# Performance work log

Measured on AMD Instinct MI355X. Metric: run time of the kernel, lower is better.

The kernel has to match this reference:

```python
import jax, jax.numpy as jnp
import numpy as np

K = 16  # num neighbors


def setup_inputs() -> dict:
    key = jax.random.key(0)
    ks = jax.random.split(key, 10)
    B, N, d_in, d_out = 4, 8192, 64, 128
    h = d_out // 2
    return {
        "xyz": jax.random.normal(ks[0], (B, 3, N), jnp.float32),
        "feature": jax.random.normal(ks[1], (B, d_in, N), jnp.float32),
        "w1": jax.random.normal(ks[2], (h, 10), jnp.float32) * 0.1,
        "b1": jax.random.normal(ks[3], (h,), jnp.float32) * 0.1,
        "w2": jax.random.normal(ks[4], (h, h), jnp.float32) * 0.1,
        "b2": jax.random.normal(ks[5], (h,), jnp.float32) * 0.1,
        "w3": jax.random.normal(ks[6], (h, h), jnp.float32) * 0.1,
        "b3": jax.random.normal(ks[7], (h,), jnp.float32) * 0.1,
        "ws": jax.random.normal(ks[8], (d_out, d_in), jnp.float32) * 0.1,
        "bs": jax.random.normal(ks[9], (d_out,), jnp.float32) * 0.1,
    }


def reference(xyz, feature, w1, b1, w2, b2, w3, b3, ws, bs):
    # xyz: [B,3,N], feature: [B,d_in,N]
    xyz_t = jnp.transpose(xyz, (0, 2, 1))  # [B,N,3]
    sq = jnp.sum(xyz_t * xyz_t, axis=-1)  # [B,N]
    # squared pairwise distance [B,N,N]
    dist = sq[:, :, None] + sq[:, None, :] - 2.0 * jnp.einsum("bnc,bmc->bnm", xyz_t, xyz_t)
    _, idx = jax.lax.top_k(-dist, K)  # smallest-k -> [B,N,K]
    # gather neighbor coords: [B,N,K,3]
    knn_xyz = jax.vmap(lambda pts, ind: pts[ind])(xyz_t, idx)
    center = jnp.broadcast_to(xyz_t[:, :, None, :], knn_xyz.shape)  # [B,N,K,3]
    diff = knn_xyz - center
    dsq = jnp.sum(diff * diff, axis=-1, keepdims=True)  # [B,N,K,1]
    pos = jnp.concatenate([center, knn_xyz, diff, dsq], axis=-1)  # [B,N,K,10]
    # three 1x1 convs over channel dim (no activations, faithful to source)
    h = jnp.einsum("bnkc,oc->bnko", pos, w1) + b1
    h = jnp.einsum("bnkc,oc->bnko", h, w2) + b2
    h = jnp.einsum("bnkc,oc->bnko", h, w3) + b3
    fe = jnp.max(h, axis=2)  # max-pool over neighbors -> [B,N,d_out//2]
    fe = jnp.transpose(fe, (0, 2, 1))  # [B,d_out//2,N]
    shortcut = jnp.einsum("bcn,oc->bon", feature, ws) + bs[None, :, None]
    return jnp.concatenate([fe, fe], axis=1) + shortcut  # [B,d_out,N]
```

## Files before the change

### kernel.cpp

```cpp
#include <hip/hip_runtime.h>

#define B_ 4
#define N_ 8192
#define DIN 64
#define HDIM 64
#define DOUT 128
#define KNN 16
#define QPB 64
#define PART 8
#define NTHR (QPB * PART)
#define CHUNK (N_ / PART)
#define CAP 16
#define BLOCKS_PER_B (N_ / QPB)

__global__ __launch_bounds__(256) void k_prep(
    const float* __restrict__ xyz,
    const float* __restrict__ w1, const float* __restrict__ b1,
    const float* __restrict__ w2, const float* __restrict__ b2,
    const float* __restrict__ w3, const float* __restrict__ b3,
    float4* __restrict__ pk, float4* __restrict__ prm) {
  const int blk = blockIdx.x, t = threadIdx.x;
  const int b = blk >> 5;
  const int m = ((blk & 31) << 8) + t;
  const float* xb = xyz + (size_t)b * 3 * N_;
  float x = xb[m], y = xb[N_ + m], z = xb[2 * N_ + m];
  float sq = __fadd_rn(__fadd_rn(__fmul_rn(x, x), __fmul_rn(y, y)), __fmul_rn(z, z));
  pk[((size_t)b << 13) + m] = make_float4(x, y, z, sq);

  if (blk == 0) {
    __shared__ float M2[HDIM][10];
    __shared__ float bb[HDIM];
    const int o = t;
    if (o < HDIM) {
      float r[10];
#pragma unroll
      for (int c = 0; c < 10; c++) r[c] = 0.f;
      float s = b2[o];
      for (int l = 0; l < HDIM; l++) {
        float w = w2[o * HDIM + l];
#pragma unroll
        for (int c = 0; c < 10; c++) r[c] = fmaf(w, w1[l * 10 + c], r[c]);
        s = fmaf(w, b1[l], s);
      }
#pragma unroll
      for (int c = 0; c < 10; c++) M2[o][c] = r[c];
      bb[o] = s;
    }
    __syncthreads();
    if (o < HDIM) {
      float r3[10];
#pragma unroll
      for (int c = 0; c < 10; c++) r3[c] = 0.f;
      float bc = b3[o];
      for (int l = 0; l < HDIM; l++) {
        float w = w3[o * HDIM + l];
#pragma unroll
        for (int c = 0; c < 10; c++) r3[c] = fmaf(w, M2[l][c], r3[c]);
        bc = fmaf(w, bb[l], bc);
      }
      prm[o]      = make_float4(r3[0] - r3[6], r3[1] - r3[7], r3[2] - r3[8], bc);
      prm[64 + o] = make_float4(r3[3] + r3[6], r3[4] + r3[7], r3[5] + r3[8], r3[9]);
    }
  }
}

#define INSERT16(VARR, IARR, VMAX, DVAL, MIDX)                    \
  {                                                               \
    bool done = false;                                            \
    _Pragma("unroll") for (int _i = 0; _i < KNN; _i++) {          \
      bool hit = (!done) && (VARR[_i] == VMAX);                   \
      if (hit) { VARR[_i] = (DVAL); IARR[_i] = (MIDX); }          \
      done = done | hit;                                          \
    }                                                             \
    float _a = fmaxf(fmaxf(fmaxf(VARR[0], VARR[1]), fmaxf(VARR[2], VARR[3])),   \
                     fmaxf(fmaxf(VARR[4], VARR[5]), fmaxf(VARR[6], VARR[7])));  \
    float _b = fmaxf(fmaxf(fmaxf(VARR[8], VARR[9]), fmaxf(VARR[10], VARR[11])), \
                     fmaxf(fmaxf(VARR[12], VARR[13]), fmaxf(VARR[14], VARR[15])));\
    VMAX = fmaxf(_a, _b);                                         \
  }

#define MAX16(VARR, VMAX)                                         \
  {                                                               \
    float _a = fmaxf(fmaxf(fmaxf(VARR[0], VARR[1]), fmaxf(VARR[2], VARR[3])),   \
                     fmaxf(fmaxf(VARR[4], VARR[5]), fmaxf(VARR[6], VARR[7])));  \
    float _b = fmaxf(fmaxf(fmaxf(VARR[8], VARR[9]), fmaxf(VARR[10], VARR[11])), \
                     fmaxf(fmaxf(VARR[12], VARR[13]), fmaxf(VARR[14], VARR[15])));\
    VMAX = fmaxf(_a, _b);                                         \
  }

#define FLUSH()                                                   \
  {                                                               \
    for (int c_ = 0; c_ < cnt; c_++) {                            \
      float fd_ = poolF[c_ * NTHR + t];                           \
      int fm_ = poolI[c_ * NTHR + t];                             \
      if (fd_ < vmax) { INSERT16(v, id, vmax, fd_, fm_); }        \
    }                                                             \
    cnt = 0;                                                      \
    atomicMin(&tau[q], __float_as_uint(vmax));                    \
    gate = fminf(vmax, __uint_as_float(tau[q]));                  \
  }

__global__ __launch_bounds__(NTHR, 4) void k_knn_fe(
    const float4* __restrict__ pk, const float4* __restrict__ prm,
    const float* __restrict__ feature, const float* __restrict__ wsM,
    const float* __restrict__ bs, float* __restrict__ out) {
  const int blk = blockIdx.x;
  const int b  = blk / BLOCKS_PER_B;
  const int n0 = (blk % BLOCKS_PER_B) * QPB;
  const int t = threadIdx.x;
  const int q = t & 63;
  const int j = __builtin_amdgcn_readfirstlane(t >> 6);

  __shared__ unsigned tau[QPB];
  __shared__ float4 prmL[2 * HDIM];
  __shared__ alignas(16) float poolF[CAP * NTHR];
  __shared__ alignas(16) unsigned short poolI[CAP * NTHR];

  if (t < QPB) tau[t] = 0x7f800000u;
  for (int i = t; i < 2 * HDIM; i += NTHR) prmL[i] = prm[i];

  const float4 qv = pk[((size_t)b << 13) + n0 + q];
  const float qx = qv.x, qy = qv.y, qz = qv.z, qs = qv.w;

  const float INF = __uint_as_float(0x7f800000u);
  float v[KNN]; int id[KNN];
  float vmax, gate;
  int cnt = 0;
  __syncthreads();

  const float4* pj = pk + ((size_t)b << 13) + j * CHUNK;

  {
    float4 c[KNN];
#pragma unroll
    for (int e = 0; e < KNN; e++) c[e] = pj[e];
#pragma unroll
    for (int e = 0; e < KNN; e++) {
      float dot = fmaf(c[e].z, qz, fmaf(c[e].y, qy, __fmul_rn(c[e].x, qx)));
      v[e] = __fsub_rn(__fadd_rn(qs, c[e].w), __fmul_rn(2.0f, dot));
      id[e] = j * CHUNK + e;
    }
    MAX16(v, vmax);
    atomicMin(&tau[q], __float_as_uint(vmax));
    gate = fminf(vmax, __uint_as_float(tau[q]));
  }

  for (int u0 = KNN; u0 < CHUNK; u0 += 8) {
    if (__any(cnt > CAP - 8)) { FLUSH(); }
    gate = fminf(gate, __uint_as_float(tau[q]));
    float4 c[8];
#pragma unroll
    for (int e = 0; e < 8; e++) c[e] = pj[u0 + e];
#pragma unroll
    for (int e = 0; e < 8; e++) {
      float dot = fmaf(c[e].z, qz, fmaf(c[e].y, qy, __fmul_rn(c[e].x, qx)));
      float d = __fsub_rn(__fadd_rn(qs, c[e].w), __fmul_rn(2.0f, dot));
      if (d < gate) {
        poolF[cnt * NTHR + t] = d;
        poolI[cnt * NTHR + t] = (unsigned short)(j * CHUNK + u0 + e);
        cnt++;
      }
    }
  }
  FLUSH();
  __syncthreads();

#pragma unroll
  for (int i = 0; i < KNN; i++) {
    poolF[(j * KNN + i) * QPB + q] = v[i];
    poolI[(j * KNN + i) * QPB + q] = (unsigned short)id[i];
  }
  __syncthreads();

  float fv[KNN]; int fid[KNN]; float fm = INF;
  if (j < 4) {
    const int l0 = (2 * j) * KNN, r1 = (2 * j + 1) * KNN;
#pragma unroll
    for (int i = 0; i < KNN; i++) {
      fv[i] = poolF[(l0 + i) * QPB + q];
      fid[i] = poolI[(l0 + i) * QPB + q];
    }
    MAX16(fv, fm);
    for (int s = 0; s < KNN; s++) {
      float d = poolF[(r1 + s) * QPB + q];
      if (d < fm) { int m_ = poolI[(r1 + s) * QPB + q]; INSERT16(fv, fid, fm, d, m_); }
    }
#pragma unroll
    for (int i = 0; i < KNN; i++) {
      poolF[(l0 + i) * QPB + q] = fv[i];
      poolI[(l0 + i) * QPB + q] = (unsigned short)fid[i];
    }
  }
  __syncthreads();
  if (j < 2) {
    const int l0 = (4 * j) * KNN, r1 = (4 * j + 2) * KNN;
#pragma unroll
    for (int i = 0; i < KNN; i++) {
      fv[i] = poolF[(l0 + i) * QPB + q];
      fid[i] = poolI[(l0 + i) * QPB + q];
    }
    MAX16(fv, fm);
    for (int s = 0; s < KNN; s++) {
      float d = poolF[(r1 + s) * QPB + q];
      if (d < fm) { int m_ = poolI[(r1 + s) * QPB + q]; INSERT16(fv, fid, fm, d, m_); }
    }
#pragma unroll
    for (int i = 0; i < KNN; i++) {
      poolF[(l0 + i) * QPB + q] = fv[i];
      poolI[(l0 + i) * QPB + q] = (unsigned short)fid[i];
    }
  }
  __syncthreads();
  if (j == 0) {
#pragma unroll
    for (int i = 0; i < KNN; i++) {
      fv[i] = poolF[i * QPB + q];
      fid[i] = poolI[i * QPB + q];
    }
    MAX16(fv, fm);
    for (int s = 0; s < KNN; s++) {
      float d = poolF[(4 * KNN + s) * QPB + q];
      if (d < fm) { int m_ = poolI[(4 * KNN + s) * QPB + q]; INSERT16(fv, fid, fm, d, m_); }
    }
#pragma unroll
    for (int i = 0; i < KNN; i++) poolI[i * QPB + q] = (unsigned short)fid[i];
  }
  __syncthreads();

#pragma unroll
  for (int kk = 0; kk < 2; kk++) {
    int k = j * 2 + kk;
    int m = poolI[k * QPB + q];
    float4 c = pk[((size_t)b << 13) + m];
    float dx = __fsub_rn(c.x, qx), dy = __fsub_rn(c.y, qy), dz = __fsub_rn(c.z, qz);
    float dsq = __fadd_rn(__fadd_rn(__fmul_rn(dx, dx), __fmul_rn(dy, dy)),
                          __fmul_rn(dz, dz));
    poolF[k * QPB + q] = c.x;
    poolF[(KNN + k) * QPB + q] = c.y;
    poolF[(2 * KNN + k) * QPB + q] = c.z;
    poolF[(3 * KNN + k) * QPB + q] = dsq;
  }
  __syncthreads();

  float fo[8];
  {
    float nx[KNN], ny[KNN], nz[KNN], nd[KNN];
#pragma unroll
    for (int k = 0; k < KNN; k++) {
      nx[k] = poolF[k * QPB + q];
      ny[k] = poolF[(KNN + k) * QPB + q];
      nz[k] = poolF[(2 * KNN + k) * QPB + q];
      nd[k] = poolF[(3 * KNN + k) * QPB + q];
    }
#pragma unroll
    for (int oi = 0; oi < 8; oi++) {
      int o = j * 8 + oi;
      float4 pA = prmL[o], pB = prmL[HDIM + o];
      float basev = fmaf(qz, pA.z, fmaf(qy, pA.y, fmaf(qx, pA.x, pA.w)));
      float mx = -INF;
#pragma unroll
      for (int k = 0; k < KNN; k++) {
        float tv = fmaf(nz[k], pB.z,
                   fmaf(ny[k], pB.y,
                   fmaf(nx[k], pB.x, __fmul_rn(nd[k], pB.w))));
        mx = fmaxf(mx, tv);
      }
      fo[oi] = basev + mx;
    }
  }
  __syncthreads();

  float* wsL = poolF;
  float* feL = (float*)poolI;
  for (int i = t; i < DOUT * DIN; i += NTHR) wsL[i] = wsM[i];
#pragma unroll
  for (int r = 0; r < 8; r++) {
    int c = j * 8 + r;
    feL[c * QPB + q] = feature[(size_t)(b * DIN + c) * N_ + n0 + q];
  }
  __syncthreads();

  float acc[16];
#pragma unroll
  for (int oi = 0; oi < 16; oi++) acc[oi] = 0.f;
  for (int c4 = 0; c4 < DIN / 4; c4++) {
    float f0 = feL[(4 * c4 + 0) * QPB + q];
    float f1 = feL[(4 * c4 + 1) * QPB + q];
    float f2 = feL[(4 * c4 + 2) * QPB + q];
    float f3 = feL[(4 * c4 + 3) * QPB + q];
#pragma unroll
    for (int oi = 0; oi < 16; oi++) {
      int o = (oi < 8) ? (j * 8 + oi) : (64 + j * 8 + oi - 8);
      float4 w = ((const float4*)(wsL + o * DIN))[c4];
      acc[oi] = fmaf(w.x, f0, acc[oi]);
      acc[oi] = fmaf(w.y, f1, acc[oi]);
      acc[oi] = fmaf(w.z, f2, acc[oi]);
      acc[oi] = fmaf(w.w, f3, acc[oi]);
    }
  }
  float* ob = out + (size_t)b * DOUT * N_ + n0 + q;
#pragma unroll
  for (int oi = 0; oi < 16; oi++) {
    int o = (oi < 8) ? (j * 8 + oi) : (64 + j * 8 + oi - 8);
    ob[(size_t)o * N_] = acc[oi] + bs[o] + fo[oi & 7];
  }
}

extern "C" void kernel_launch(void* const* d_in, const int* in_sizes, int n_in,
                              void* d_out, int out_size, void* d_ws, size_t ws_size,
                              hipStream_t stream) {
  const float* xyz     = (const float*)d_in[0];
  const float* feature = (const float*)d_in[1];
  const float* w1 = (const float*)d_in[2];
  const float* b1 = (const float*)d_in[3];
  const float* w2 = (const float*)d_in[4];
  const float* b2 = (const float*)d_in[5];
  const float* w3 = (const float*)d_in[6];
  const float* b3 = (const float*)d_in[7];
  const float* wsM = (const float*)d_in[8];
  const float* bs  = (const float*)d_in[9];
  float* out = (float*)d_out;

  float4* prm = (float4*)d_ws;
  float4* pkB = (float4*)((char*)d_ws + 8192);

  hipLaunchKernelGGL(k_prep, dim3(128), dim3(256), 0, stream,
                     xyz, w1, b1, w2, b2, w3, b3, pkB, prm);
  hipLaunchKernelGGL(k_knn_fe, dim3(B_ * BLOCKS_PER_B), dim3(NTHR), 0, stream,
                     pkB, prm, feature, wsM, bs, out);
}
```

Baseline: 286.5 us.

## Stage candidate tiles into LDS via async global_load_lds and use cheaper pre-filter

Candidate points are now streamed per partition into double-buffered LDS tiles with global_load_lds, prefetching the next tile while the current one is scanned, in place of direct global loads. Each candidate gets a cheap three-FMA pre-filter, c.w - 2*q·c compared against gate - qs plus a small margin. The exact rounded distance is computed only for candidates that pass. The per-group tau refresh of the gate is dropped, so the gate only tightens at flushes, and the extra LDS raises shared memory use, which may lower occupancy.

```diff
diff --git a/kernel.cpp b/kernel.cpp
--- a/kernel.cpp
+++ b/kernel.cpp
@@ -11,7 +11,15 @@
 #define NTHR (QPB * PART)
 #define CHUNK (N_ / PART)
 #define CAP 16
+#define TILE 64
+#define NT (CHUNK / TILE)
 #define BLOCKS_PER_B (N_ / QPB)
+#define GMARGIN 1e-3f
+
+#define GL2LDS(gp, lp)                                             \
+  __builtin_amdgcn_global_load_lds(                                \
+      (const __attribute__((address_space(1))) void*)(gp),         \
+      (__attribute__((address_space(3))) void*)(lp), 16, 0, 0)
 
 __global__ __launch_bounds__(256) void k_prep(
     const float* __restrict__ xyz,
@@ -98,6 +106,7 @@
     cnt = 0;                                                      \
     atomicMin(&tau[q], __float_as_uint(vmax));                    \
     gate = fminf(vmax, __uint_as_float(tau[q]));                  \
+    G = __fadd_rn(__fsub_rn(gate, qs), GMARGIN);                  \
   }
 
 __global__ __launch_bounds__(NTHR, 4) void k_knn_fe(
@@ -115,20 +124,24 @@
   __shared__ float4 prmL[2 * HDIM];
   __shared__ alignas(16) float poolF[CAP * NTHR];
   __shared__ alignas(16) unsigned short poolI[CAP * NTHR];
+  __shared__ alignas(16) float4 tiles[PART][2][TILE];
 
   if (t < QPB) tau[t] = 0x7f800000u;
   for (int i = t; i < 2 * HDIM; i += NTHR) prmL[i] = prm[i];
 
   const float4 qv = pk[((size_t)b << 13) + n0 + q];
   const float qx = qv.x, qy = qv.y, qz = qv.z, qs = qv.w;
+  const float nx2 = -2.0f * qx, ny2 = -2.0f * qy, nz2 = -2.0f * qz;
 
   const float INF = __uint_as_float(0x7f800000u);
   float v[KNN]; int id[KNN];
-  float vmax, gate;
+  float vmax, gate, G;
   int cnt = 0;
   __syncthreads();
 
   const float4* pj = pk + ((size_t)b << 13) + j * CHUNK;
+
+  GL2LDS(pj + q, &tiles[j][0][0]);
 
   {
     float4 c[KNN];
@@ -143,22 +156,34 @@
     MAX16(v, vmax);
     atomicMin(&tau[q], __float_as_uint(vmax));
     gate = fminf(vmax, __uint_as_float(tau[q]));
-  }
-
-  for (int u0 = KNN; u0 < CHUNK; u0 += 8) {
-    if (__any(cnt > CAP - 8)) { FLUSH(); }
-    gate = fminf(gate, __uint_as_float(tau[q]));
-    float4 c[8];
-#pragma unroll
-    for (int e = 0; e < 8; e++) c[e] = pj[u0 + e];
-#pragma unroll
-    for (int e = 0; e < 8; e++) {
-      float dot = fmaf(c[e].z, qz, fmaf(c[e].y, qy, __fmul_rn(c[e].x, qx)));
-      float d = __fsub_rn(__fadd_rn(qs, c[e].w), __fmul_rn(2.0f, dot));
-      if (d < gate) {
-        poolF[cnt * NTHR + t] = d;
-        poolI[cnt * NTHR + t] = (unsigned short)(j * CHUNK + u0 + e);
-        cnt++;
+    G = __fadd_rn(__fsub_rn(gate, qs), GMARGIN);
+  }
+
+  for (int T = 0; T < NT; T++) {
+    if (T + 1 < NT) {
+      GL2LDS(pj + (T + 1) * TILE + q, &tiles[j][(T + 1) & 1][0]);
+      asm volatile("s_waitcnt vmcnt(1)" ::: "memory");
+    } else {
+      asm volatile("s_waitcnt vmcnt(0)" ::: "memory");
+    }
+    const float4* tb = &tiles[j][T & 1][0];
+    const int m0 = j * CHUNK + T * TILE;
+    const int g0 = (T == 0) ? 2 : 0;
+    for (int gr = g0; gr < TILE / 8; gr++) {
+      if (__any(cnt > CAP - 8)) { FLUSH(); }
+      float4 c[8];
+#pragma unroll
+      for (int e = 0; e < 8; e++) c[e] = tb[gr * 8 + e];
+#pragma unroll
+      for (int e = 0; e < 8; e++) {
+        float gg = fmaf(c[e].x, nx2, fmaf(c[e].y, ny2, fmaf(c[e].z, nz2, c[e].w)));
+        if (gg < G) {
+          float dot = fmaf(c[e].z, qz, fmaf(c[e].y, qy, __fmul_rn(c[e].x, qx)));
+          float d = __fsub_rn(__fadd_rn(qs, c[e].w), __fmul_rn(2.0f, dot));
+          poolF[cnt * NTHR + t] = d;
+          poolI[cnt * NTHR + t] = (unsigned short)(m0 + gr * 8 + e);
+          cnt++;
+        }
       }
     }
   }
```

New measurement: 293.9 us. 2.6% more time.
